# Optimization experiments

Measured on AMD Instinct MI355X. Metric: run time of the kernel, lower is better.

## Reference

```python
import jax, jax.numpy as jnp
import numpy as np
import math

N_HEADS = 16

def _layernorm(x, g, b):
    m = x.mean(-1, keepdims=True)
    v = ((x - m) ** 2).mean(-1, keepdims=True)
    return (x - m) * jax.lax.rsqrt(v + 1e-5) * g + b

def _project(x):
    # Poincare ball (c=1) projection: clip last-dim norm to 1 - eps
    max_norm = 1.0 - 1e-5
    n = jnp.linalg.norm(x, axis=-1, keepdims=True)
    return jnp.where(n > max_norm, x * (max_norm / jnp.maximum(n, 1e-12)), x)


def setup_inputs() -> dict:
    key = jax.random.key(0)
    ks = jax.random.split(key, 8)
    B, L, D = 2, 2048, 1024
    w = lambda k, s: jax.random.normal(k, s, jnp.float32) * 0.02
    return dict(
        x=jax.random.normal(ks[0], (B, L, D), jnp.float32),
        wq=w(ks[1], (D, D)), bq=jnp.zeros((D,), jnp.float32),
        wk=w(ks[2], (D, D)), bk=jnp.zeros((D,), jnp.float32),
        wv=w(ks[3], (D, D)), bv=jnp.zeros((D,), jnp.float32),
        wo=w(ks[4], (D, D)), bo=jnp.zeros((D,), jnp.float32),
        g1=jnp.ones((D,), jnp.float32), b1=jnp.zeros((D,), jnp.float32),
        g2=jnp.ones((D,), jnp.float32), b2=jnp.zeros((D,), jnp.float32),
        w1=w(ks[5], (4 * D, D)), bf1=jnp.zeros((4 * D,), jnp.float32),
        w2=w(ks[6], (D, 4 * D)), bf2=jnp.zeros((D,), jnp.float32),
    )


def reference(x, wq, bq, wk, bk, wv, bv, wo, bo, g1, b1, g2, b2, w1, bf1, w2, bf2):
    B, L, D = x.shape
    H = N_HEADS
    hd = D // H
    temp = math.sqrt(hd)

    xn = _layernorm(x, g1, b1)

    def heads(w, b):
        y = xn @ w.T + b                       # [B, L, D]
        return y.reshape(B, L, H, hd).transpose(0, 2, 1, 3)  # [B, H, L, hd]

    q = _project(heads(wq, bq))
    k = _project(heads(wk, bk))
    v = heads(wv, bv)

    # -||q - k||^2 / temp, via ||q||^2 + ||k||^2 - 2 q.k (same math as the
    # explicit broadcast-diff in the torch code, expressed as a GEMM)
    q2 = (q ** 2).sum(-1)[..., :, None]        # [B, H, L, 1]
    k2 = (k ** 2).sum(-1)[..., None, :]        # [B, H, 1, L]
    qk = jnp.einsum('bhld,bhmd->bhlm', q, k)   # [B, H, L, L]
    scores = -(q2 + k2 - 2.0 * qk) / temp
    attn = jax.nn.softmax(scores, axis=-1)     # dropout = identity (eval mode)

    out = jnp.einsum('bhlm,bhmd->bhld', attn, v)
    out = out.transpose(0, 2, 1, 3).reshape(B, L, D) @ wo.T + bo

    x = _project(x + out)
    xn2 = _layernorm(x, g2, b2)
    h = jax.nn.gelu(xn2 @ w1.T + bf1, approximate=False)  # torch nn.GELU = erf
    x = _project(x + (h @ w2.T + bf2))
    return x
```

## Files before the change

### kernel.cpp

```cpp
#include <hip/hip_runtime.h>
#include <math.h>

#define SEQ_L 2048
#define DM    1024
#define NH    16
#define HD    64
#define BL    4096
#define DFF   4096
#define QKV_S 3072

typedef __attribute__((ext_vector_type(8))) short short8;
typedef __attribute__((ext_vector_type(4))) short s16x4;
typedef __attribute__((ext_vector_type(4))) float f32x4;

__device__ __forceinline__ short f2bf(float x) {
    unsigned u = __float_as_uint(x);
    u += 0x7fff + ((u >> 16) & 1);
    return (short)(u >> 16);
}
__device__ __forceinline__ float bf2f(short s) {
    return __uint_as_float(((unsigned)(unsigned short)s) << 16);
}

__device__ __forceinline__ float gelu_fast(float x) {
    const float xa = fabsf(x);
    const float z = xa * 0.70710678118654752440f;
    const float t = __builtin_amdgcn_rcpf(fmaf(0.3275911f, z, 1.f));
    float P = fmaf(t, 1.061405429f, -1.453152027f);
    P = fmaf(t, P, 1.421413741f);
    P = fmaf(t, P, -0.284496736f);
    P = fmaf(t, P, 0.254829592f);
    P *= t;
    const float e = __expf(-z * z);
    const float erfp = fmaf(-P, e, 1.f);
    return 0.5f * fmaf(xa, erfp, x);
}

__device__ __forceinline__ float block_sum(float v, float* red, int tid) {
#pragma unroll
    for (int m = 32; m; m >>= 1) v += __shfl_xor(v, m);
    if ((tid & 63) == 0) red[tid >> 6] = v;
    __syncthreads();
    v = red[0] + red[1] + red[2] + red[3];
    __syncthreads();
    return v;
}

__global__ __launch_bounds__(256) void cvt6_kernel(
    const float* __restrict__ wq, const float* __restrict__ wk,
    const float* __restrict__ wv, const float* __restrict__ wo,
    const float* __restrict__ w1, const float* __restrict__ w2,
    short* __restrict__ dst) {
    const size_t i = (size_t)blockIdx.x * 256 + threadIdx.x;
    const float* src;
    size_t off;
    if (i < 1048576) {
        const int seg = (int)(i >> 18);
        off = i & 262143;
        src = seg == 0 ? wq : seg == 1 ? wk : seg == 2 ? wv : wo;
    } else if (i < 2097152) { src = w1; off = i - 1048576; }
    else                    { src = w2; off = i - 2097152; }
    const float4 v = ((const float4*)src)[off];
    const s16x4 o = {f2bf(v.x), f2bf(v.y), f2bf(v.z), f2bf(v.w)};
    ((s16x4*)dst)[i] = o;
}

__global__ __launch_bounds__(256) void ln_bf16_kernel(const float* __restrict__ x,
                                                      const float* __restrict__ g,
                                                      const float* __restrict__ b,
                                                      short* __restrict__ out) {
    const int row = blockIdx.x;
    const int tid = threadIdx.x;
    __shared__ float red[4];
    const float4 xv = *(const float4*)(x + (size_t)row * DM + tid * 4);
    float s = xv.x + xv.y + xv.z + xv.w;
    s = block_sum(s, red, tid);
    const float mean = s * (1.f / (float)DM);
    float dx0 = xv.x - mean, dx1 = xv.y - mean, dx2 = xv.z - mean, dx3 = xv.w - mean;
    float ss = dx0 * dx0 + dx1 * dx1 + dx2 * dx2 + dx3 * dx3;
    ss = block_sum(ss, red, tid);
    const float rs = 1.f / sqrtf(ss * (1.f / (float)DM) + 1e-5f);
    const float4 gv = *(const float4*)(g + tid * 4);
    const float4 bv = *(const float4*)(b + tid * 4);
    const s16x4 ob = {f2bf(dx0 * rs * gv.x + bv.x), f2bf(dx1 * rs * gv.y + bv.y),
                      f2bf(dx2 * rs * gv.z + bv.z), f2bf(dx3 * rs * gv.w + bv.w)};
    *(s16x4*)(out + (size_t)row * DM + tid * 4) = ob;
}

__global__ __launch_bounds__(256) void resproj_kernel(const float* __restrict__ a,
                                                      const float* __restrict__ c,
                                                      float* __restrict__ out) {
    const int row = blockIdx.x;
    const int tid = threadIdx.x;
    __shared__ float red[4];
    const float4 av = *(const float4*)(a + (size_t)row * DM + tid * 4);
    const float4 cv = *(const float4*)(c + (size_t)row * DM + tid * 4);
    float4 sv;
    sv.x = av.x + cv.x; sv.y = av.y + cv.y; sv.z = av.z + cv.z; sv.w = av.w + cv.w;
    float ss = sv.x * sv.x + sv.y * sv.y + sv.z * sv.z + sv.w * sv.w;
    ss = block_sum(ss, red, tid);
    const float n = sqrtf(ss);
    const float mx = 1.f - 1e-5f;
    const float scale = (n > mx) ? (mx / fmaxf(n, 1e-12f)) : 1.f;
    sv.x *= scale; sv.y *= scale; sv.z *= scale; sv.w *= scale;
    *(float4*)(out + (size_t)row * DM + tid * 4) = sv;
}

__global__ __launch_bounds__(256) void qk_prep(const short* __restrict__ qkvB,
                                               short* __restrict__ Qb,
                                               short* __restrict__ Kb,
                                               float* __restrict__ k2) {
    const int tid = threadIdx.x, lane = tid & 63;
    const int vec = blockIdx.x * 4 + (tid >> 6);
    const int row = vec >> 4, h = vec & 15;
    const int b = row >> 11, l = row & 2047;
    const size_t dstv = ((size_t)(b * NH + h) * SEQ_L + l) * HD + lane;
    const float mx = 1.f - 1e-5f;
    {
        const float v = bf2f(qkvB[(size_t)row * QKV_S + h * HD + lane]);
        float s = v * v;
#pragma unroll
        for (int m = 32; m; m >>= 1) s += __shfl_xor(s, m);
        const float n = sqrtf(s);
        const float sc = (n > mx) ? (mx / fmaxf(n, 1e-12f)) : 1.f;
        Qb[dstv] = f2bf(v * sc);
    }
    {
        const float v = bf2f(qkvB[(size_t)row * QKV_S + DM + h * HD + lane]);
        float s = v * v;
#pragma unroll
        for (int m = 32; m; m >>= 1) s += __shfl_xor(s, m);
        const float n = sqrtf(s);
        const float sc = (n > mx) ? (mx / fmaxf(n, 1e-12f)) : 1.f;
        Kb[dstv] = f2bf(v * sc);
        if (lane == 0) k2[(size_t)(b * NH + h) * SEQ_L + l] = s * sc * sc * 0.125f;
    }
}

__global__ __launch_bounds__(256) void v_prep(const short* __restrict__ qkvB,
                                              short* __restrict__ Vtb) {
    const int blk = blockIdx.x;
    const int bh = blk >> 5, kt = blk & 31;
    const int b = bh >> 4, h = bh & 15;
    __shared__ short T[64 * 72];
    const int tid = threadIdx.x;
    {
        const int key = tid >> 2, ch = (tid & 3) * 16;
        const size_t src = ((size_t)b * SEQ_L + kt * 64 + key) * QKV_S + 2 * DM + h * HD + ch;
        *(short8*)&T[key * 72 + ch]     = *(const short8*)(qkvB + src);
        *(short8*)&T[key * 72 + ch + 8] = *(const short8*)(qkvB + src + 8);
    }
    __syncthreads();
    const int hd = tid >> 2, kc = (tid & 3) * 16;
    short8 o0, o1;
#pragma unroll
    for (int j = 0; j < 8; ++j) {
        o0[j] = T[(kc + j) * 72 + hd];
        o1[j] = T[(kc + 8 + j) * 72 + hd];
    }
    short* dst = Vtb + ((size_t)bh * HD + hd) * SEQ_L + kt * 64 + kc;
    *(short8*)dst = o0;
    *(short8*)(dst + 8) = o1;
}

template <int BM, int ACT, int OUTBF, int FUSED>
__global__ __launch_bounds__(256) void gemm_mfma(
    const short* __restrict__ A, const short* __restrict__ Bw,
    const float* __restrict__ bb0, const float* __restrict__ bb1,
    const float* __restrict__ bb2, void* __restrict__ Cout,
    int M, int N, int K) {
    constexpr int RT = BM / 32;
    constexpr bool VEPI = (OUTBF != 0) && (BM == 128);
    constexpr int SMEM_BYTES = VEPI ? (4 * 64 * 72 * 2) : ((BM * 32 + 128 * 32) * 2);
    __shared__ __align__(16) char raw[SMEM_BYTES];
    short* As = (short*)raw;
    short* Bs = As + BM * 32;
    const int tid = threadIdx.x;
    const int wv = tid >> 6, lane = tid & 63;
    const int m0 = blockIdx.y * BM, n0 = blockIdx.x * 128;
    const int wr = (wv & 1) * (BM / 2);
    const int wc = (wv >> 1) * 64;

    const int arow = wv * (BM / 4) + (lane >> 2);
    const int brow = wv * 32 + (lane >> 2);
    const short* Ag = A + (size_t)(m0 + arow) * K + (lane & 3) * 8;
    const short* Bg = Bw + (size_t)(n0 + brow) * K + (lane & 3) * 8;
    short* AsW = As + (wv * (BM / 4)) * 32 + lane * 8;
    short* AsW2 = AsW + 16 * 32;
    short* BsW = Bs + (wv * 32) * 32 + lane * 8;
    short* BsW2 = BsW + 16 * 32;

    const f32x4 z4 = {0.f, 0.f, 0.f, 0.f};
    f32x4 acc[RT][4];
#pragma unroll
    for (int r = 0; r < RT; ++r)
#pragma unroll
        for (int c = 0; c < 4; ++c) acc[r][c] = z4;

    const int lrow = lane & 15, kq = (lane >> 4) * 8;

    short8 ra0, ra1, rb0, rb1;
    ra0 = *(const short8*)(Ag);
    if constexpr (BM == 128) ra1 = *(const short8*)(Ag + (size_t)16 * K);
    rb0 = *(const short8*)(Bg);
    rb1 = *(const short8*)(Bg + (size_t)16 * K);

    for (int kt = 0; kt < K; kt += 32) {
        __syncthreads();
        *(short8*)AsW = ra0;
        if constexpr (BM == 128) *(short8*)AsW2 = ra1;
        *(short8*)BsW = rb0;
        *(short8*)BsW2 = rb1;
        short8 na0, na1, nb0, nb1;
        if (kt + 32 < K) {
            na0 = *(const short8*)(Ag + kt + 32);
            if constexpr (BM == 128) na1 = *(const short8*)(Ag + (size_t)16 * K + kt + 32);
            nb0 = *(const short8*)(Bg + kt + 32);
            nb1 = *(const short8*)(Bg + (size_t)16 * K + kt + 32);
        }
        __syncthreads();
        short8 af[RT], bf[4];
#pragma unroll
        for (int r = 0; r < RT; ++r)
            af[r] = *(const short8*)&As[(wr + r * 16 + lrow) * 32 + kq];
#pragma unroll
        for (int c = 0; c < 4; ++c)
            bf[c] = *(const short8*)&Bs[(wc + c * 16 + lrow) * 32 + kq];
#pragma unroll
        for (int r = 0; r < RT; ++r)
#pragma unroll
            for (int c = 0; c < 4; ++c)
                acc[r][c] = __builtin_amdgcn_mfma_f32_16x16x32_bf16(af[r], bf[c], acc[r][c], 0, 0, 0);
        ra0 = na0; ra1 = na1; rb0 = nb0; rb1 = nb1;
    }

    const int col = lane & 15, rb = (lane >> 4) * 4;
    if constexpr (VEPI) {
        __syncthreads();
        short* Ot = (short*)raw + wv * (64 * 72);
#pragma unroll
        for (int c = 0; c < 4; ++c) {
            const int gn = n0 + wc + c * 16 + col;
            float bias;
            if constexpr (FUSED) {
                const int seg = gn >> 10;
                bias = (seg == 0 ? bb0 : seg == 1 ? bb1 : bb2)[gn & 1023];
            } else {
                bias = bb0[gn];
            }
#pragma unroll
            for (int r = 0; r < RT; ++r)
#pragma unroll
                for (int i = 0; i < 4; ++i) {
                    float v = acc[r][c][i] + bias;
                    if constexpr (ACT) v = gelu_fast(v);
                    Ot[(r * 16 + rb + i) * 72 + c * 16 + col] = f2bf(v);
                }
        }
        const int orow = lane >> 3, oc = (lane & 7) * 8;
#pragma unroll
        for (int it = 0; it < 8; ++it) {
            const short8 vv = *(const short8*)&Ot[(it * 8 + orow) * 72 + oc];
            *(short8*)((short*)Cout + (size_t)(m0 + wr + it * 8 + orow) * N + n0 + wc + oc) = vv;
        }
    } else {
#pragma unroll
        for (int c = 0; c < 4; ++c) {
            const int gn = n0 + wc + c * 16 + col;
            float bias;
            if constexpr (FUSED) {
                const int seg = gn >> 10;
                bias = (seg == 0 ? bb0 : seg == 1 ? bb1 : bb2)[gn & 1023];
            } else {
                bias = bb0[gn];
            }
#pragma unroll
            for (int r = 0; r < RT; ++r) {
                const int gm = m0 + wr + r * 16 + rb;
#pragma unroll
                for (int i = 0; i < 4; ++i) {
                    float v = acc[r][c][i] + bias;
                    if constexpr (ACT) v = gelu_fast(v);
                    if constexpr (OUTBF)
                        ((short*)Cout)[(size_t)(gm + i) * N + gn] = f2bf(v);
                    else
                        ((float*)Cout)[(size_t)(gm + i) * N + gn] = v;
                }
            }
        }
    }
}

__global__ __launch_bounds__(256) void attn_mfma2(const short* __restrict__ Qb,
                                                  const short* __restrict__ Kb,
                                                  const short* __restrict__ Vtb,
                                                  const float* __restrict__ k2v,
                                                  short* __restrict__ aO) {
    const int qt = blockIdx.x, h = blockIdx.y, b = blockIdx.z;
    const int tid = threadIdx.x, wv = tid >> 6, lane = tid & 63;
    const int bh = b * NH + h;
    __shared__ __align__(16) short smem[2 * 64 * 72];
    short* Ks = smem;
    short* Vt = smem + 64 * 72;
    const int lrow = lane & 15, q8 = (lane >> 4) * 8, q4 = (lane >> 4) * 4;

    const short* Qh = Qb + (size_t)bh * SEQ_L * HD;
    const short* Kh = Kb + (size_t)bh * SEQ_L * HD;
    const short* Vh = Vtb + (size_t)bh * HD * SEQ_L;
    const float* k2p = k2v + (size_t)bh * SEQ_L;

    short8 qf[2][2];
#pragma unroll
    for (int nt = 0; nt < 2; ++nt)
#pragma unroll
        for (int kc = 0; kc < 2; ++kc)
            qf[nt][kc] = *(const short8*)(Qh +
                (size_t)(qt * 128 + wv * 32 + nt * 16 + lrow) * HD + kc * 32 + q8);

    const f32x4 z4 = {0.f, 0.f, 0.f, 0.f};
    f32x4 o[4][2];
#pragma unroll
    for (int ht = 0; ht < 4; ++ht)
#pragma unroll
        for (int nt = 0; nt < 2; ++nt) o[ht][nt] = z4;
    float lsum[2] = {0.f, 0.f};

    const int srow = tid >> 2, sch = (tid & 3) * 16;

    for (int kt = 0; kt < SEQ_L / 64; ++kt) {
        const int k0 = kt * 64;
        __syncthreads();
        {
            const short* g = Kh + (size_t)(k0 + srow) * HD + sch;
            *(short8*)&Ks[srow * 72 + sch]     = *(const short8*)g;
            *(short8*)&Ks[srow * 72 + sch + 8] = *(const short8*)(g + 8);
            const short* gv = Vh + (size_t)srow * SEQ_L + k0 + sch;
            *(short8*)&Vt[srow * 72 + sch]     = *(const short8*)gv;
            *(short8*)&Vt[srow * 72 + sch + 8] = *(const short8*)(gv + 8);
        }
        __syncthreads();

        short8 p8[2][2];
#pragma unroll
        for (int mt = 0; mt < 4; ++mt) {
            const short8 kf0 = *(const short8*)&Ks[(mt * 16 + lrow) * 72 + q8];
            const short8 kf1 = *(const short8*)&Ks[(mt * 16 + lrow) * 72 + 32 + q8];
            const float4 kk = *(const float4*)(k2p + k0 + mt * 16 + q4);
            const int c = mt >> 1, hi = (mt & 1) * 4;
#pragma unroll
            for (int nt = 0; nt < 2; ++nt) {
                f32x4 s = z4;
                s = __builtin_amdgcn_mfma_f32_16x16x32_bf16(kf0, qf[nt][0], s, 0, 0, 0);
                s = __builtin_amdgcn_mfma_f32_16x16x32_bf16(kf1, qf[nt][1], s, 0, 0, 0);
#pragma unroll
                for (int i = 0; i < 4; ++i) {
                    const float kki = (i == 0) ? kk.x : (i == 1) ? kk.y : (i == 2) ? kk.z : kk.w;
                    const float p = __expf(fmaf(s[i], 0.25f, -kki));
                    lsum[nt] += p;
                    p8[nt][c][hi + i] = f2bf(p);
                }
            }
        }
#pragma unroll
        for (int ht = 0; ht < 4; ++ht) {
#pragma unroll
            for (int c = 0; c < 2; ++c) {
                const s16x4 va = *(const s16x4*)&Vt[(ht * 16 + lrow) * 72 + c * 32 + q4];
                const s16x4 vb = *(const s16x4*)&Vt[(ht * 16 + lrow) * 72 + c * 32 + 16 + q4];
                const short8 v8 = {va[0], va[1], va[2], va[3], vb[0], vb[1], vb[2], vb[3]};
#pragma unroll
                for (int nt = 0; nt < 2; ++nt)
                    o[ht][nt] = __builtin_amdgcn_mfma_f32_16x16x32_bf16(v8, p8[nt][c], o[ht][nt], 0, 0, 0);
            }
        }
    }

#pragma unroll
    for (int nt = 0; nt < 2; ++nt) {
        lsum[nt] += __shfl_xor(lsum[nt], 16);
        lsum[nt] += __shfl_xor(lsum[nt], 32);
    }
    const float inv0 = 1.f / lsum[0], inv1 = 1.f / lsum[1];

    __syncthreads();
    short* Ot = smem + wv * (32 * 72);
#pragma unroll
    for (int ht = 0; ht < 4; ++ht)
#pragma unroll
        for (int nt = 0; nt < 2; ++nt) {
            const float iv = nt ? inv1 : inv0;
            const s16x4 ov = {f2bf(o[ht][nt][0] * iv), f2bf(o[ht][nt][1] * iv),
                              f2bf(o[ht][nt][2] * iv), f2bf(o[ht][nt][3] * iv)};
            *(s16x4*)&Ot[(nt * 16 + lrow) * 72 + ht * 16 + q4] = ov;
        }
    const int erow = lane >> 1, ec = (lane & 1) * 32;
    const short8 r0 = *(const short8*)&Ot[erow * 72 + ec + 0];
    const short8 r1 = *(const short8*)&Ot[erow * 72 + ec + 8];
    const short8 r2 = *(const short8*)&Ot[erow * 72 + ec + 16];
    const short8 r3 = *(const short8*)&Ot[erow * 72 + ec + 24];
    short* dst = aO + ((size_t)b * SEQ_L + qt * 128 + wv * 32 + erow) * DM + h * HD + ec;
    *(short8*)(dst + 0)  = r0;
    *(short8*)(dst + 8)  = r1;
    *(short8*)(dst + 16) = r2;
    *(short8*)(dst + 24) = r3;
}

extern "C" void kernel_launch(void* const* d_in, const int* in_sizes, int n_in,
                              void* d_out, int out_size, void* d_ws, size_t ws_size,
                              hipStream_t stream) {
    const float* x   = (const float*)d_in[0];
    const float* wq  = (const float*)d_in[1];
    const float* bq  = (const float*)d_in[2];
    const float* wk  = (const float*)d_in[3];
    const float* bk  = (const float*)d_in[4];
    const float* wv  = (const float*)d_in[5];
    const float* bv  = (const float*)d_in[6];
    const float* wo  = (const float*)d_in[7];
    const float* bo  = (const float*)d_in[8];
    const float* g1  = (const float*)d_in[9];
    const float* b1  = (const float*)d_in[10];
    const float* g2  = (const float*)d_in[11];
    const float* b2  = (const float*)d_in[12];
    const float* w1  = (const float*)d_in[13];
    const float* bf1 = (const float*)d_in[14];
    const float* w2  = (const float*)d_in[15];
    const float* bf2 = (const float*)d_in[16];
    float* out = (float*)d_out;

    char* base = (char*)d_ws;
    short* wbf  = (short*)base;
    short* qkvB = (short*)(base + (24u << 20));
    short* xnb  = (short*)(base + (48u << 20));
    short* Qb   = xnb;
    short* Kb   = (short*)(base + (56u << 20));
    short* Vtb  = (short*)(base + (64u << 20));
    float* k2   = (float*)(base + (72u << 20));
    short* aO   = (short*)(base + (72u << 20) + (256u << 10));
    float* P    = (float*)(base + (24u << 20));
    short* xn2b = Vtb;
    short* hbuf = qkvB;
    float* y2   = (float*)(base + (58u << 20));

    cvt6_kernel<<<12288, 256, 0, stream>>>(wq, wk, wv, wo, w1, w2, wbf);
    ln_bf16_kernel<<<BL, 256, 0, stream>>>(x, g1, b1, xnb);
    gemm_mfma<128, 0, 1, 1><<<dim3(24, 32), 256, 0, stream>>>(
        xnb, wbf, bq, bk, bv, qkvB, BL, QKV_S, DM);
    qk_prep<<<16384, 256, 0, stream>>>(qkvB, Qb, Kb, k2);
    v_prep<<<1024, 256, 0, stream>>>(qkvB, Vtb);
    attn_mfma2<<<dim3(16, 16, 2), 256, 0, stream>>>(Qb, Kb, Vtb, k2, aO);
    gemm_mfma<64, 0, 0, 0><<<dim3(8, 64), 256, 0, stream>>>(
        aO, wbf + 3145728, bo, bo, bo, P, BL, DM, DM);
    resproj_kernel<<<BL, 256, 0, stream>>>(x, P, out);
    ln_bf16_kernel<<<BL, 256, 0, stream>>>(out, g2, b2, xn2b);
    gemm_mfma<128, 1, 1, 0><<<dim3(32, 32), 256, 0, stream>>>(
        xn2b, wbf + 4194304, bf1, bf1, bf1, hbuf, BL, DFF, DM);
    gemm_mfma<64, 0, 0, 0><<<dim3(8, 64), 256, 0, stream>>>(
        hbuf, wbf + 8388608, bf2, bf2, bf2, y2, BL, DM, DFF);
    resproj_kernel<<<BL, 256, 0, stream>>>(out, y2, out);
}
```

Before: 400.1 us.

## Split-K the N=1024 GEMMs with BM=128 and pad LDS rows

New measurement: 769.8 us. 1.92x slower.

```diff
diff --git a/kernel.cpp b/kernel.cpp
--- a/kernel.cpp
+++ b/kernel.cpp
@@ -106,6 +106,28 @@
     *(float4*)(out + (size_t)row * DM + tid * 4) = sv;
 }
 
+__global__ __launch_bounds__(256) void resproj2_kernel(const float* __restrict__ a,
+                                                       const float* __restrict__ c0,
+                                                       const float* __restrict__ c1,
+                                                       float* __restrict__ out) {
+    const int row = blockIdx.x;
+    const int tid = threadIdx.x;
+    __shared__ float red[4];
+    const float4 av = *(const float4*)(a + (size_t)row * DM + tid * 4);
+    const float4 cv = *(const float4*)(c0 + (size_t)row * DM + tid * 4);
+    const float4 dv = *(const float4*)(c1 + (size_t)row * DM + tid * 4);
+    float4 sv;
+    sv.x = av.x + cv.x + dv.x; sv.y = av.y + cv.y + dv.y;
+    sv.z = av.z + cv.z + dv.z; sv.w = av.w + cv.w + dv.w;
+    float ss = sv.x * sv.x + sv.y * sv.y + sv.z * sv.z + sv.w * sv.w;
+    ss = block_sum(ss, red, tid);
+    const float n = sqrtf(ss);
+    const float mx = 1.f - 1e-5f;
+    const float scale = (n > mx) ? (mx / fmaxf(n, 1e-12f)) : 1.f;
+    sv.x *= scale; sv.y *= scale; sv.z *= scale; sv.w *= scale;
+    *(float4*)(out + (size_t)row * DM + tid * 4) = sv;
+}
+
 __global__ __launch_bounds__(256) void qk_prep(const short* __restrict__ qkvB,
                                                short* __restrict__ Qb,
                                                short* __restrict__ Kb,
@@ -163,32 +185,39 @@
     *(short8*)(dst + 8) = o1;
 }
 
-template <int BM, int ACT, int OUTBF, int FUSED>
+template <int BM, int ACT, int OUTBF, int FUSED, int SPLITK>
 __global__ __launch_bounds__(256) void gemm_mfma(
     const short* __restrict__ A, const short* __restrict__ Bw,
     const float* __restrict__ bb0, const float* __restrict__ bb1,
     const float* __restrict__ bb2, void* __restrict__ Cout,
+    void* __restrict__ Cout2,
     int M, int N, int K) {
     constexpr int RT = BM / 32;
+    constexpr int LDSR = 36;
     constexpr bool VEPI = (OUTBF != 0) && (BM == 128);
-    constexpr int SMEM_BYTES = VEPI ? (4 * 64 * 72 * 2) : ((BM * 32 + 128 * 32) * 2);
+    constexpr int STAGE_BYTES = (BM + 128) * LDSR * 2;
+    constexpr int SMEM_BYTES = VEPI ? (4 * 64 * 72 * 2) : STAGE_BYTES;
+    static_assert(!VEPI || SMEM_BYTES >= STAGE_BYTES, "VEPI smem too small");
     __shared__ __align__(16) char raw[SMEM_BYTES];
     short* As = (short*)raw;
-    short* Bs = As + BM * 32;
+    short* Bs = As + BM * LDSR;
     const int tid = threadIdx.x;
     const int wv = tid >> 6, lane = tid & 63;
     const int m0 = blockIdx.y * BM, n0 = blockIdx.x * 128;
     const int wr = (wv & 1) * (BM / 2);
     const int wc = (wv >> 1) * 64;
 
+    const int z = (SPLITK > 1) ? blockIdx.z : 0;
+    const int Kc = K / SPLITK;
+
     const int arow = wv * (BM / 4) + (lane >> 2);
     const int brow = wv * 32 + (lane >> 2);
-    const short* Ag = A + (size_t)(m0 + arow) * K + (lane & 3) * 8;
-    const short* Bg = Bw + (size_t)(n0 + brow) * K + (lane & 3) * 8;
-    short* AsW = As + (wv * (BM / 4)) * 32 + lane * 8;
-    short* AsW2 = AsW + 16 * 32;
-    short* BsW = Bs + (wv * 32) * 32 + lane * 8;
-    short* BsW2 = BsW + 16 * 32;
+    const short* Ag = A + (size_t)(m0 + arow) * K + z * Kc + (lane & 3) * 8;
+    const short* Bg = Bw + (size_t)(n0 + brow) * K + z * Kc + (lane & 3) * 8;
+    short* AsW = As + (wv * (BM / 4) + (lane >> 2)) * LDSR + (lane & 3) * 8;
+    short* AsW2 = AsW + 16 * LDSR;
+    short* BsW = Bs + (wv * 32 + (lane >> 2)) * LDSR + (lane & 3) * 8;
+    short* BsW2 = BsW + 16 * LDSR;
 
     const f32x4 z4 = {0.f, 0.f, 0.f, 0.f};
     f32x4 acc[RT][4];
@@ -205,14 +234,14 @@
     rb0 = *(const short8*)(Bg);
     rb1 = *(const short8*)(Bg + (size_t)16 * K);
 
-    for (int kt = 0; kt < K; kt += 32) {
+    for (int kt = 0; kt < Kc; kt += 32) {
         __syncthreads();
         *(short8*)AsW = ra0;
         if constexpr (BM == 128) *(short8*)AsW2 = ra1;
         *(short8*)BsW = rb0;
         *(short8*)BsW2 = rb1;
         short8 na0, na1, nb0, nb1;
-        if (kt + 32 < K) {
+        if (kt + 32 < Kc) {
             na0 = *(const short8*)(Ag + kt + 32);
             if constexpr (BM == 128) na1 = *(const short8*)(Ag + (size_t)16 * K + kt + 32);
             nb0 = *(const short8*)(Bg + kt + 32);
@@ -222,10 +251,10 @@
         short8 af[RT], bf[4];
 #pragma unroll
         for (int r = 0; r < RT; ++r)
-            af[r] = *(const short8*)&As[(wr + r * 16 + lrow) * 32 + kq];
+            af[r] = *(const short8*)&As[(wr + r * 16 + lrow) * LDSR + kq];
 #pragma unroll
         for (int c = 0; c < 4; ++c)
-            bf[c] = *(const short8*)&Bs[(wc + c * 16 + lrow) * 32 + kq];
+            bf[c] = *(const short8*)&Bs[(wc + c * 16 + lrow) * LDSR + kq];
 #pragma unroll
         for (int r = 0; r < RT; ++r)
 #pragma unroll
@@ -233,6 +262,9 @@
                 acc[r][c] = __builtin_amdgcn_mfma_f32_16x16x32_bf16(af[r], bf[c], acc[r][c], 0, 0, 0);
         ra0 = na0; ra1 = na1; rb0 = nb0; rb1 = nb1;
     }
+
+    void* Cbase = Cout;
+    if constexpr (SPLITK > 1) { if (z) Cbase = Cout2; }
 
     const int col = lane & 15, rb = (lane >> 4) * 4;
     if constexpr (VEPI) {
@@ -261,7 +293,7 @@
 #pragma unroll
         for (int it = 0; it < 8; ++it) {
             const short8 vv = *(const short8*)&Ot[(it * 8 + orow) * 72 + oc];
-            *(short8*)((short*)Cout + (size_t)(m0 + wr + it * 8 + orow) * N + n0 + wc + oc) = vv;
+            *(short8*)((short*)Cbase + (size_t)(m0 + wr + it * 8 + orow) * N + n0 + wc + oc) = vv;
         }
     } else {
 #pragma unroll
@@ -274,6 +306,7 @@
             } else {
                 bias = bb0[gn];
             }
+            if constexpr (SPLITK > 1) { if (z) bias = 0.f; }
 #pragma unroll
             for (int r = 0; r < RT; ++r) {
                 const int gm = m0 + wr + r * 16 + rb;
@@ -282,9 +315,9 @@
                     float v = acc[r][c][i] + bias;
                     if constexpr (ACT) v = gelu_fast(v);
                     if constexpr (OUTBF)
-                        ((short*)Cout)[(size_t)(gm + i) * N + gn] = f2bf(v);
+                        ((short*)Cbase)[(size_t)(gm + i) * N + gn] = f2bf(v);
                     else
-                        ((float*)Cout)[(size_t)(gm + i) * N + gn] = v;
+                        ((float*)Cbase)[(size_t)(gm + i) * N + gn] = v;
                 }
             }
         }
@@ -437,24 +470,26 @@
     float* k2   = (float*)(base + (72u << 20));
     short* aO   = (short*)(base + (72u << 20) + (256u << 10));
     float* P    = (float*)(base + (24u << 20));
+    float* P2   = (float*)(base + (40u << 20));
     short* xn2b = Vtb;
     short* hbuf = qkvB;
-    float* y2   = (float*)(base + (58u << 20));
+    float* y0   = (float*)base;
+    float* y1   = (float*)(base + (56u << 20));
 
     cvt6_kernel<<<12288, 256, 0, stream>>>(wq, wk, wv, wo, w1, w2, wbf);
     ln_bf16_kernel<<<BL, 256, 0, stream>>>(x, g1, b1, xnb);
-    gemm_mfma<128, 0, 1, 1><<<dim3(24, 32), 256, 0, stream>>>(
-        xnb, wbf, bq, bk, bv, qkvB, BL, QKV_S, DM);
+    gemm_mfma<128, 0, 1, 1, 1><<<dim3(24, 32), 256, 0, stream>>>(
+        xnb, wbf, bq, bk, bv, qkvB, nullptr, BL, QKV_S, DM);
     qk_prep<<<16384, 256, 0, stream>>>(qkvB, Qb, Kb, k2);
     v_prep<<<1024, 256, 0, stream>>>(qkvB, Vtb);
     attn_mfma2<<<dim3(16, 16, 2), 256, 0, stream>>>(Qb, Kb, Vtb, k2, aO);
-    gemm_mfma<64, 0, 0, 0><<<dim3(8, 64), 256, 0, stream>>>(
-        aO, wbf + 3145728, bo, bo, bo, P, BL, DM, DM);
-    resproj_kernel<<<BL, 256, 0, stream>>>(x, P, out);
+    gemm_mfma<128, 0, 0, 0, 2><<<dim3(8, 32, 2), 256, 0, stream>>>(
+        aO, wbf + 3145728, bo, bo, bo, P, P2, BL, DM, DM);
+    resproj2_kernel<<<BL, 256, 0, stream>>>(x, P, P2, out);
     ln_bf16_kernel<<<BL, 256, 0, stream>>>(out, g2, b2, xn2b);
-    gemm_mfma<128, 1, 1, 0><<<dim3(32, 32), 256, 0, stream>>>(
-        xn2b, wbf + 4194304, bf1, bf1, bf1, hbuf, BL, DFF, DM);
-    gemm_mfma<64, 0, 0, 0><<<dim3(8, 64), 256, 0, stream>>>(
-        hbuf, wbf + 8388608, bf2, bf2, bf2, y2, BL, DM, DFF);
-    resproj_kernel<<<BL, 256, 0, stream>>>(out, y2, out);
-}
+    gemm_mfma<128, 1, 1, 0, 1><<<dim3(32, 32), 256, 0, stream>>>(
+        xn2b, wbf + 4194304, bf1, bf1, bf1, hbuf, nullptr, BL, DFF, DM);
+    gemm_mfma<128, 0, 0, 0, 2><<<dim3(8, 32, 2), 256, 0, stream>>>(
+        hbuf, wbf + 8388608, bf2, bf2, bf2, y0, y1, BL, DM, DFF);
+    resproj2_kernel<<<BL, 256, 0, stream>>>(out, y0, y1, out);
+}
```
